# Optimization experiments

Measured on AMD Instinct MI355X. Metric: run time of the kernel, lower is better.

The kernel has to match this reference:

```python
import jax, jax.numpy as jnp
import numpy as np

B, S, DIN, D, H, DOUT, W = 4, 2048, 256, 512, 8, 128, 64
HD = D // H


def setup_inputs() -> dict:
    key = jax.random.key(0)
    ks = jax.random.split(key, 16)
    r = lambda k, shape, s=0.02: (jax.random.normal(k, shape, jnp.float32) * s)
    return dict(
        x=jax.random.normal(ks[0], (B, S, DIN), jnp.float32),
        pos=jax.random.normal(ks[1], (1, S, D), jnp.float32),  # torch.randn init
        win_w=r(ks[2], (DIN, D)), win_b=jnp.zeros((D,), jnp.float32),
        l_wqkv=r(ks[3], (3, D, D)), l_bqkv=jnp.zeros((3, D), jnp.float32),
        l_wo=r(ks[4], (D, D)), l_bo=jnp.zeros((D,), jnp.float32),
        g_wqkv=r(ks[5], (3, D, D)), g_bqkv=jnp.zeros((3, D), jnp.float32),
        g_wo=r(ks[6], (D, D)), g_bo=jnp.zeros((D,), jnp.float32),
        gate_w=r(ks[7], (2 * D, D)), gate_b=jnp.zeros((D,), jnp.float32),
        ffn_w1=r(ks[8], (D, 2 * D)), ffn_b1=jnp.zeros((2 * D,), jnp.float32),
        ffn_w2=r(ks[9], (2 * D, D)), ffn_b2=jnp.zeros((D,), jnp.float32),
        n1_g=jnp.ones((D,), jnp.float32), n1_b=jnp.zeros((D,), jnp.float32),
        n2_g=jnp.ones((D,), jnp.float32), n2_b=jnp.zeros((D,), jnp.float32),
        n3_g=jnp.ones((D,), jnp.float32), n3_b=jnp.zeros((D,), jnp.float32),
        out_w=r(ks[10], (D, DOUT)), out_b=jnp.zeros((DOUT,), jnp.float32),
    )


def _ln(x, g, b, eps=1e-5):
    m = x.mean(-1, keepdims=True)
    v = ((x - m) ** 2).mean(-1, keepdims=True)
    return (x - m) * jax.lax.rsqrt(v + eps) * g + b


def _mha(x, wqkv, bqkv, wo, bo, mask):
    b, s, d = x.shape
    q = (x @ wqkv[0] + bqkv[0]).reshape(b, s, H, HD)
    k = (x @ wqkv[1] + bqkv[1]).reshape(b, s, H, HD)
    v = (x @ wqkv[2] + bqkv[2]).reshape(b, s, H, HD)
    scores = jnp.einsum('bqhd,bkhd->bhqk', q, k) / np.sqrt(HD).astype(np.float32)
    if mask is not None:
        scores = scores + mask  # additive -inf band mask
    attn = jax.nn.softmax(scores, axis=-1)
    o = jnp.einsum('bhqk,bkhd->bqhd', attn, v).reshape(b, s, d)
    return o @ wo + bo


def reference(x, pos, win_w, win_b,
              l_wqkv, l_bqkv, l_wo, l_bo,
              g_wqkv, g_bqkv, g_wo, g_bo,
              gate_w, gate_b, ffn_w1, ffn_b1, ffn_w2, ffn_b2,
              n1_g, n1_b, n2_g, n2_b, n3_g, n3_b, out_w, out_b):
    s = x.shape[1]
    # band mask: row i allows cols [i - W//2, i + W//2] (matches create_local_mask)
    idx = jnp.arange(s)
    band = jnp.abs(idx[:, None] - idx[None, :]) <= (W // 2)
    mask = jnp.where(band, 0.0, -jnp.inf).astype(jnp.float32)

    h = x @ win_w + win_b + pos
    local_out = _mha(h, l_wqkv, l_bqkv, l_wo, l_bo, mask)
    global_out = _mha(h, g_wqkv, g_bqkv, g_wo, g_bo, None)

    combined = jnp.concatenate([local_out, global_out], axis=-1)
    gate = jnp.tanh(jax.nn.relu(combined @ gate_w + gate_b))
    fused = gate * local_out + (1.0 - gate) * global_out

    h = _ln(h + fused, n1_g, n1_b)
    ffn = jax.nn.relu(h @ ffn_w1 + ffn_b1) @ ffn_w2 + ffn_b2
    h = _ln(h + ffn, n2_g, n2_b)
    h = _ln(h, n3_g, n3_b)
    pooled = h.mean(axis=1)  # AdaptiveAvgPool1d(1) over seq
    return pooled @ out_w + out_b
```

## Files before the change

kernel.cpp:

```cpp
#include <hip/hip_runtime.h>
#include <math.h>
#include <stdint.h>

#define S_LEN 2048
#define DMODEL 512
#define NHEAD 8
#define BATCH 4
#define M_ROWS (BATCH * S_LEN)
#define UAC 4194304

typedef __attribute__((ext_vector_type(8))) short frag8;
typedef __attribute__((ext_vector_type(4))) float f32x4;

__device__ inline unsigned short f2bf(float f) {
    unsigned int u = __float_as_uint(f);
    return (unsigned short)((u + 0x7FFFu + ((u >> 16) & 1u)) >> 16);
}
__device__ inline float bf2f(unsigned short h) {
    return __uint_as_float(((unsigned int)h) << 16);
}

#if __has_builtin(__builtin_amdgcn_exp2f)
#define EXP2(x) __builtin_amdgcn_exp2f(x)
#else
#define EXP2(x) __expf(0.6931471805599453f * (x))
#endif

#if __has_builtin(__builtin_amdgcn_global_load_lds)
__device__ __forceinline__ void glds16(const void* g, void* l, int lane) {
    __builtin_amdgcn_global_load_lds(
        (__attribute__((address_space(1))) void*)(uintptr_t)g,
        (__attribute__((address_space(3))) void*)(uintptr_t)l, 16, 0, 0);
    (void)lane;
}
#else
__device__ __forceinline__ void glds16(const void* g, void* l, int lane) {
    ((uint4*)l)[lane] = ((const uint4*)g)[0];
}
#endif

struct WSeg { const float* src; unsigned short* dst; int K; int N; int start; };
struct WTab { WSeg s[12]; };

__global__ __launch_bounds__(256) void wcast_all(WTab tab)
{
    __shared__ float t[32][33];
    const int bid = blockIdx.x;
    int si = 0;
#pragma unroll
    for (int i = 1; i < 12; ++i) if (bid >= tab.s[i].start) si = i;
    const WSeg sg = tab.s[si];
    const int tile = bid - sg.start;
    const int nk = sg.K >> 5;
    const int k0 = (tile % nk) * 32, n0 = (tile / nk) * 32;
    {
        int kk = threadIdx.x >> 3, nq = (threadIdx.x & 7) * 4;
        float4 v = *(const float4*)&sg.src[(size_t)(k0 + kk) * sg.N + n0 + nq];
        t[kk][nq + 0] = v.x; t[kk][nq + 1] = v.y; t[kk][nq + 2] = v.z; t[kk][nq + 3] = v.w;
    }
    __syncthreads();
    {
        int n = threadIdx.x >> 3, kq = (threadIdx.x & 7) * 4;
        ushort4 o;
        o.x = f2bf(t[kq + 0][n]); o.y = f2bf(t[kq + 1][n]);
        o.z = f2bf(t[kq + 2][n]); o.w = f2bf(t[kq + 3][n]);
        *(ushort4*)&sg.dst[(size_t)(n0 + n) * sg.K + k0 + kq] = o;
    }
}

__global__ __launch_bounds__(256) void castx_kernel(
    const float* __restrict__ x, unsigned short* __restrict__ xb)
{
    const size_t i = ((size_t)blockIdx.x * 256 + threadIdx.x) * 8;
    float4 a = *(const float4*)&x[i], b = *(const float4*)&x[i + 4];
    unsigned short us[8];
    us[0] = f2bf(a.x); us[1] = f2bf(a.y); us[2] = f2bf(a.z); us[3] = f2bf(a.w);
    us[4] = f2bf(b.x); us[5] = f2bf(b.y); us[6] = f2bf(b.z); us[7] = f2bf(b.w);
    *(uint4*)&xb[i] = *(uint4*)us;
}

__global__ __launch_bounds__(256) void vtrans_kernel(
    const unsigned short* __restrict__ V, unsigned short* __restrict__ Vt)
{
    __shared__ unsigned short T[64][72];
    const int st = blockIdx.x, bh = blockIdx.y;
    const int b = bh >> 3, h = bh & 7;
    const int tid = threadIdx.x;
    {
        const int s = tid >> 2, d0 = (tid & 3) * 16;
        const unsigned short* src = V + ((size_t)(b * S_LEN + st * 64 + s) * DMODEL + h * 64 + d0);
        *(uint4*)&T[s][d0] = *(const uint4*)src;
        *(uint4*)&T[s][d0 + 8] = *(const uint4*)(src + 8);
    }
    __syncthreads();
    {
        const int d = tid >> 2, s0 = (tid & 3) * 16;
        unsigned short buf[16];
#pragma unroll
        for (int j = 0; j < 16; ++j) buf[j] = T[s0 + j][d];
        unsigned short* dst = Vt + ((size_t)(bh * 64 + d) * S_LEN + st * 64 + s0);
        *(uint4*)&dst[0] = *(const uint4*)&buf[0];
        *(uint4*)&dst[8] = *(const uint4*)&buf[8];
    }
}

template <int MODE, int BN>
__global__ __launch_bounds__(256) void gemm_mfma(
    const unsigned short* __restrict__ A, const unsigned short* __restrict__ A2,
    const unsigned short* __restrict__ Wt, const float* __restrict__ bias,
    const float* __restrict__ pos, unsigned short* __restrict__ C,
    int M, int N, int K)
{
    constexpr int UN = BN / 32;
    __shared__ unsigned short As[128 * 64];
    __shared__ unsigned short Bs[BN * 64];
    const int tid = threadIdx.x;
    const int wave = tid >> 6, lane = tid & 63;
    const int lr = lane & 15, quad = lane >> 4;
    const int bm = blockIdx.x * 128, bn = blockIdx.y * BN;
    const int rm = (wave >> 1) * 64, rn = (wave & 1) * (BN / 2);
    const int Khalf = K >> 1;
    const int KA = (MODE == 3) ? Khalf : K;

    const int lrow = lane >> 3;
    const int gch = ((lane & 7) - lrow) & 7;
    const size_t laneA = (size_t)(bm + wave * 32 + lrow) * KA + gch * 8;
    const size_t laneB = (size_t)(bn + wave * (BN / 4) + lrow) * K + gch * 8;
    unsigned short* ldsA = As + wave * 2048;
    unsigned short* ldsB = Bs + wave * (BN * 16);

    f32x4 acc[4][UN];
#pragma unroll
    for (int t = 0; t < 4; ++t)
#pragma unroll
        for (int u = 0; u < UN; ++u) acc[t][u] = (f32x4){0.f, 0.f, 0.f, 0.f};

    const int sw0 = ((quad + lr) & 7) * 8;
    const int sw1 = ((quad + lr + 4) & 7) * 8;

    for (int k0 = 0; k0 < K; k0 += 64) {
        __syncthreads();
        const unsigned short* Ab; int kadj;
        if constexpr (MODE == 3) { Ab = (k0 < Khalf) ? A : A2; kadj = k0 & (Khalf - 1); }
        else { Ab = A; kadj = k0; }
        const unsigned short* pa = Ab + laneA + kadj;
        glds16(pa,           ldsA,        lane);
        glds16(pa + 8 * KA,  ldsA + 512,  lane);
        glds16(pa + 16 * KA, ldsA + 1024, lane);
        glds16(pa + 24 * KA, ldsA + 1536, lane);
        const unsigned short* pb = Wt + laneB + k0;
#pragma unroll
        for (int i = 0; i < UN; ++i)
            glds16(pb + i * 8 * K, ldsB + i * 512, lane);
        __syncthreads();

#pragma unroll
        for (int kc = 0; kc < 2; ++kc) {
            const int sw = kc ? sw1 : sw0;
            frag8 af[4], bf[UN];
#pragma unroll
            for (int t = 0; t < 4; ++t)
                af[t] = *(const frag8*)&As[(rm + t * 16 + lr) * 64 + sw];
#pragma unroll
            for (int u = 0; u < UN; ++u)
                bf[u] = *(const frag8*)&Bs[(rn + u * 16 + lr) * 64 + sw];
#pragma unroll
            for (int t = 0; t < 4; ++t)
#pragma unroll
                for (int u = 0; u < UN; ++u)
                    acc[t][u] = __builtin_amdgcn_mfma_f32_16x16x32_bf16(
                        af[t], bf[u], acc[t][u], 0, 0, 0);
        }
    }

#pragma unroll
    for (int t = 0; t < 4; ++t) {
#pragma unroll
        for (int i = 0; i < 4; ++i) {
            const int m = bm + rm + t * 16 + quad * 4 + i;
#pragma unroll
            for (int u = 0; u < UN; ++u) {
                const int n = bn + rn + u * 16 + lr;
                float v = acc[t][u][i] + bias[n];
                if constexpr (MODE == 1) v += pos[(size_t)(m & (S_LEN - 1)) * N + n];
                if constexpr (MODE == 2) v = fmaxf(v, 0.0f);
                if constexpr (MODE == 3) {
                    float g = tanhf(fmaxf(v, 0.0f));
                    float lo = bf2f(A[(size_t)m * Khalf + n]);
                    float go = bf2f(A2[(size_t)m * Khalf + n]);
                    v = g * lo + (1.0f - g) * go;
                }
                if constexpr (MODE == 5) {
                    const int mat = n >> 9;
                    if (mat == 0) v *= 0.18033688011112042f;
                    C[(size_t)mat * UAC + (size_t)m * DMODEL + (n & 511)] = f2bf(v);
                } else {
                    C[(size_t)m * N + n] = f2bf(v);
                }
            }
        }
    }
}

__global__ __launch_bounds__(256) void attn_mfma(
    const unsigned short* __restrict__ Q, const unsigned short* __restrict__ Kv,
    const unsigned short* __restrict__ Vt, unsigned short* __restrict__ O, int masked)
{
    __shared__ unsigned short Ks[64 * 64];
    __shared__ unsigned short Vts[64 * 64];
    __shared__ unsigned short Ps[64][72];
    const int qt = blockIdx.x, h = blockIdx.y, b = blockIdx.z;
    const int tid = threadIdx.x;
    const int wave = tid >> 6, lane = tid & 63;
    const int lr = lane & 15, quad = lane >> 4, q8 = quad * 8;

    {
        const int q = tid >> 2, d0 = (tid & 3) * 16;
        const unsigned short* src = Q + ((size_t)(b * S_LEN + qt * 64 + q) * DMODEL + h * 64 + d0);
        *(uint4*)&Ps[q][d0] = *(const uint4*)src;
        *(uint4*)&Ps[q][d0 + 8] = *(const uint4*)(src + 8);
    }
    frag8 qf[2];
    qf[0] = *(const frag8*)&Ps[wave * 16 + lr][q8];
    qf[1] = *(const frag8*)&Ps[wave * 16 + lr][32 + q8];

    f32x4 oacc[4];
#pragma unroll
    for (int t = 0; t < 4; ++t) oacc[t] = (f32x4){0.f, 0.f, 0.f, 0.f};
    float l_r = 0.f;

    int kt0 = 0, kt1 = S_LEN / 64 - 1;
    if (masked) { kt0 = qt > 0 ? qt - 1 : 0; kt1 = qt < 31 ? qt + 1 : 31; }

    const int lrow = lane >> 3;
    const int gch = ((lane & 7) - lrow) & 7;
    const unsigned short* kp = Kv + ((size_t)(b * S_LEN + kt0 * 64 + wave * 16 + lrow) * DMODEL + h * 64 + gch * 8);
    const unsigned short* vp = Vt + ((size_t)((b * 8 + h) * 64 + wave * 16 + lrow) * S_LEN + kt0 * 64 + gch * 8);
    unsigned short* lk = Ks + wave * 1024;
    unsigned short* lv = Vts + wave * 1024;

    const int sw0 = ((quad + lr) & 7) * 8;
    const int sw1 = ((quad + lr + 4) & 7) * 8;

    for (int kt = kt0; kt <= kt1; ++kt) {
        __syncthreads();
        glds16(kp, lk, lane);
        glds16(kp + 8 * DMODEL, lk + 512, lane);
        glds16(vp, lv, lane);
        glds16(vp + 8 * S_LEN, lv + 512, lane);
        kp += 64 * DMODEL; vp += 64;
        __syncthreads();

        f32x4 sacc[4];
#pragma unroll
        for (int t = 0; t < 4; ++t) sacc[t] = (f32x4){0.f, 0.f, 0.f, 0.f};
#pragma unroll
        for (int kc = 0; kc < 2; ++kc) {
            const int sw = kc ? sw1 : sw0;
#pragma unroll
            for (int t = 0; t < 4; ++t) {
                frag8 kf = *(const frag8*)&Ks[(t * 16 + lr) * 64 + sw];
                sacc[t] = __builtin_amdgcn_mfma_f32_16x16x32_bf16(kf, qf[kc], sacc[t], 0, 0, 0);
            }
        }

#pragma unroll
        for (int t = 0; t < 4; ++t) {
            float p0 = EXP2(sacc[t][0]);
            float p1 = EXP2(sacc[t][1]);
            float p2 = EXP2(sacc[t][2]);
            float p3 = EXP2(sacc[t][3]);
            if (masked) {
                const int qa = qt * 64 + wave * 16 + lr;
                const int ca = kt * 64 + t * 16 + quad * 4;
                int d0 = qa - ca;
                if (d0 > 32 || d0 < -32) p0 = 0.f;
                int d1 = qa - (ca + 1);
                if (d1 > 32 || d1 < -32) p1 = 0.f;
                int d2 = qa - (ca + 2);
                if (d2 > 32 || d2 < -32) p2 = 0.f;
                int d3 = qa - (ca + 3);
                if (d3 > 32 || d3 < -32) p3 = 0.f;
            }
            const unsigned u0 = __float_as_uint(p0) & 0xFFFF0000u;
            const unsigned u1 = __float_as_uint(p1) & 0xFFFF0000u;
            const unsigned u2 = __float_as_uint(p2) & 0xFFFF0000u;
            const unsigned u3 = __float_as_uint(p3) & 0xFFFF0000u;
            l_r += (__uint_as_float(u0) + __uint_as_float(u1)) +
                   (__uint_as_float(u2) + __uint_as_float(u3));
            uint2 pw;
            pw.x = __builtin_amdgcn_perm(u1, u0, 0x07060302);
            pw.y = __builtin_amdgcn_perm(u3, u2, 0x07060302);
            *(uint2*)&Ps[wave * 16 + lr][t * 16 + quad * 4] = pw;
        }

#pragma unroll
        for (int cc = 0; cc < 2; ++cc) {
            frag8 pa = *(const frag8*)&Ps[wave * 16 + lr][cc * 32 + q8];
            const int sw = cc ? sw1 : sw0;
#pragma unroll
            for (int t = 0; t < 4; ++t) {
                frag8 vf = *(const frag8*)&Vts[(t * 16 + lr) * 64 + sw];
                oacc[t] = __builtin_amdgcn_mfma_f32_16x16x32_bf16(pa, vf, oacc[t], 0, 0, 0);
            }
        }
    }

    l_r += __shfl_xor(l_r, 16);
    l_r += __shfl_xor(l_r, 32);
#pragma unroll
    for (int i = 0; i < 4; ++i) {
        const float inv = 1.0f / __shfl(l_r, quad * 4 + i);
        const int q = qt * 64 + wave * 16 + quad * 4 + i;
#pragma unroll
        for (int t = 0; t < 4; ++t)
            O[(size_t)(b * S_LEN + q) * DMODEL + h * 64 + t * 16 + lr] = f2bf(oacc[t][i] * inv);
    }
}

__device__ inline float wave_sum64(float v) {
#pragma unroll
    for (int off = 1; off < 64; off <<= 1) v += __shfl_xor(v, off);
    return v;
}

__global__ __launch_bounds__(256) void ln_res_kernel(
    const unsigned short* __restrict__ A, const unsigned short* __restrict__ Bb,
    const float* __restrict__ g, const float* __restrict__ be,
    unsigned short* __restrict__ out)
{
    const size_t row = blockIdx.x * 4 + (threadIdx.x >> 6);
    const int lane = threadIdx.x & 63;
    float x[8]; float s = 0.f;
#pragma unroll
    for (int k = 0; k < 8; ++k) {
        size_t idx = row * DMODEL + k * 64 + lane;
        x[k] = bf2f(A[idx]) + bf2f(Bb[idx]);
        s += x[k];
    }
    s = wave_sum64(s);
    float mean = s * (1.0f / DMODEL);
    float v = 0.f;
#pragma unroll
    for (int k = 0; k < 8; ++k) { float d = x[k] - mean; v += d * d; }
    v = wave_sum64(v) * (1.0f / DMODEL);
    float r = rsqrtf(v + 1e-5f);
#pragma unroll
    for (int k = 0; k < 8; ++k)
        out[row * DMODEL + k * 64 + lane] =
            f2bf((x[k] - mean) * r * g[k * 64 + lane] + be[k * 64 + lane]);
}

__global__ __launch_bounds__(256) void ln_double_kernel(
    const unsigned short* __restrict__ A, const unsigned short* __restrict__ Bb,
    const float* __restrict__ g2, const float* __restrict__ b2,
    const float* __restrict__ g3, const float* __restrict__ b3,
    unsigned short* __restrict__ out)
{
    const size_t row = blockIdx.x * 4 + (threadIdx.x >> 6);
    const int lane = threadIdx.x & 63;
    float x[8]; float s = 0.f;
#pragma unroll
    for (int k = 0; k < 8; ++k) {
        size_t idx = row * DMODEL + k * 64 + lane;
        x[k] = bf2f(A[idx]) + bf2f(Bb[idx]);
        s += x[k];
    }
    s = wave_sum64(s);
    float mean = s * (1.0f / DMODEL);
    float v = 0.f;
#pragma unroll
    for (int k = 0; k < 8; ++k) { float d = x[k] - mean; v += d * d; }
    v = wave_sum64(v) * (1.0f / DMODEL);
    float r = rsqrtf(v + 1e-5f);
    float t[8]; float s2 = 0.f;
#pragma unroll
    for (int k = 0; k < 8; ++k) {
        t[k] = (x[k] - mean) * r * g2[k * 64 + lane] + b2[k * 64 + lane];
        s2 += t[k];
    }
    s2 = wave_sum64(s2);
    float mean2 = s2 * (1.0f / DMODEL);
    float v2 = 0.f;
#pragma unroll
    for (int k = 0; k < 8; ++k) { float d = t[k] - mean2; v2 += d * d; }
    v2 = wave_sum64(v2) * (1.0f / DMODEL);
    float r2 = rsqrtf(v2 + 1e-5f);
#pragma unroll
    for (int k = 0; k < 8; ++k)
        out[row * DMODEL + k * 64 + lane] =
            f2bf((t[k] - mean2) * r2 * g3[k * 64 + lane] + b3[k * 64 + lane]);
}

__global__ __launch_bounds__(256) void pool_kernel(
    const unsigned short* __restrict__ h2, float* __restrict__ pooled)
{
    const int b = blockIdx.x >> 4;
    const int chunk = blockIdx.x & 15;
    const int tid = threadIdx.x;
    float s0 = 0.f, s1 = 0.f;
    size_t base = (size_t)(b * S_LEN + chunk * 128) * DMODEL;
    for (int r = 0; r < 128; ++r) {
        s0 += bf2f(h2[base + (size_t)r * DMODEL + tid]);
        s1 += bf2f(h2[base + (size_t)r * DMODEL + 256 + tid]);
    }
    atomicAdd(&pooled[b * DMODEL + tid], s0);
    atomicAdd(&pooled[b * DMODEL + 256 + tid], s1);
}

__global__ __launch_bounds__(128) void out_kernel(
    const float* __restrict__ pooled, const float* __restrict__ w,
    const float* __restrict__ bias, float* __restrict__ out)
{
    const int b = blockIdx.x;
    const int o = threadIdx.x;
    float acc = 0.f;
    for (int d = 0; d < DMODEL; ++d)
        acc += pooled[b * DMODEL + d] * w[d * 128 + o];
    out[b * 128 + o] = acc * (1.0f / S_LEN) + bias[o];
}

extern "C" void kernel_launch(void* const* d_in, const int* in_sizes, int n_in,
                              void* d_out, int out_size, void* d_ws, size_t ws_size,
                              hipStream_t stream)
{
    const float* x      = (const float*)d_in[0];
    const float* pos    = (const float*)d_in[1];
    const float* win_w  = (const float*)d_in[2];
    const float* win_b  = (const float*)d_in[3];
    const float* l_wqkv = (const float*)d_in[4];
    const float* l_bqkv = (const float*)d_in[5];
    const float* l_wo   = (const float*)d_in[6];
    const float* l_bo   = (const float*)d_in[7];
    const float* g_wqkv = (const float*)d_in[8];
    const float* g_bqkv = (const float*)d_in[9];
    const float* g_wo   = (const float*)d_in[10];
    const float* g_bo   = (const float*)d_in[11];
    const float* gate_w = (const float*)d_in[12];
    const float* gate_b = (const float*)d_in[13];
    const float* ffn_w1 = (const float*)d_in[14];
    const float* ffn_b1 = (const float*)d_in[15];
    const float* ffn_w2 = (const float*)d_in[16];
    const float* ffn_b2 = (const float*)d_in[17];
    const float* n1_g   = (const float*)d_in[18];
    const float* n1_b   = (const float*)d_in[19];
    const float* n2_g   = (const float*)d_in[20];
    const float* n2_b   = (const float*)d_in[21];
    const float* n3_g   = (const float*)d_in[22];
    const float* n3_b   = (const float*)d_in[23];
    const float* out_w  = (const float*)d_in[24];
    const float* out_b  = (const float*)d_in[25];
    float* out = (float*)d_out;

    unsigned short* ws16 = (unsigned short*)d_ws;
    const size_t UA = (size_t)UAC;
    unsigned short* H  = ws16 + 0 * UA;
    unsigned short* Qb = ws16 + 1 * UA;
    unsigned short* Kb = ws16 + 2 * UA;
    unsigned short* Vb = ws16 + 3 * UA;
    unsigned short* AO = ws16 + 4 * UA;
    unsigned short* LO = ws16 + 5 * UA;
    unsigned short* VT = ws16 + 6 * UA;
    unsigned short* GO     = Qb;
    unsigned short* FUSED  = Kb;
    unsigned short* H1     = Vb;
    unsigned short* FFNMID = AO;
    unsigned short* FFNOUT = Qb;
    unsigned short* H2     = Kb;
    float* POOLED = (float*)(void*)H;

    unsigned short* wt = ws16 + 7 * UA;
    unsigned short* win_t  = wt;
    unsigned short* lqkv_t = win_t  + 131072;
    unsigned short* lwo_t  = lqkv_t + 786432;
    unsigned short* gqkv_t = lwo_t  + 262144;
    unsigned short* gwo_t  = gqkv_t + 786432;
    unsigned short* gate_t = gwo_t  + 262144;
    unsigned short* ffn1_t = gate_t + 524288;
    unsigned short* ffn2_t = ffn1_t + 524288;
    unsigned short* xb     = ffn2_t + 524288;

    WTab tab;
    tab.s[0]  = {win_w,             win_t,             256,  512,    0};
    tab.s[1]  = {l_wqkv + 0*262144, lqkv_t + 0*262144, 512,  512,  128};
    tab.s[2]  = {l_wqkv + 1*262144, lqkv_t + 1*262144, 512,  512,  384};
    tab.s[3]  = {l_wqkv + 2*262144, lqkv_t + 2*262144, 512,  512,  640};
    tab.s[4]  = {l_wo,              lwo_t,             512,  512,  896};
    tab.s[5]  = {g_wqkv + 0*262144, gqkv_t + 0*262144, 512,  512, 1152};
    tab.s[6]  = {g_wqkv + 1*262144, gqkv_t + 1*262144, 512,  512, 1408};
    tab.s[7]  = {g_wqkv + 2*262144, gqkv_t + 2*262144, 512,  512, 1664};
    tab.s[8]  = {g_wo,              gwo_t,             512,  512, 1920};
    tab.s[9]  = {gate_w,            gate_t,            1024, 512, 2176};
    tab.s[10] = {ffn_w1,            ffn1_t,            512, 1024, 2688};
    tab.s[11] = {ffn_w2,            ffn2_t,            1024, 512, 3200};

    dim3 blk(256);
    wcast_all<<<dim3(3712), blk, 0, stream>>>(tab);
    castx_kernel<<<dim3(1024), blk, 0, stream>>>(x, xb);

    dim3 gD(M_ROWS / 128, 512 / 64);
    dim3 gQ(M_ROWS / 128, 1536 / 128);
    dim3 gF(M_ROWS / 128, 1024 / 128);
    dim3 gA(S_LEN / 64, NHEAD, BATCH);
    dim3 gV(S_LEN / 64, BATCH * NHEAD);

    gemm_mfma<1, 64><<<gD, blk, 0, stream>>>(xb, nullptr, win_t, win_b, pos, H, M_ROWS, 512, 256);

    gemm_mfma<5, 128><<<gQ, blk, 0, stream>>>(H, nullptr, lqkv_t, l_bqkv, nullptr, Qb, M_ROWS, 1536, 512);
    vtrans_kernel<<<gV, blk, 0, stream>>>(Vb, VT);
    attn_mfma<<<gA, blk, 0, stream>>>(Qb, Kb, VT, AO, 1);
    gemm_mfma<0, 64><<<gD, blk, 0, stream>>>(AO, nullptr, lwo_t, l_bo, nullptr, LO, M_ROWS, 512, 512);

    gemm_mfma<5, 128><<<gQ, blk, 0, stream>>>(H, nullptr, gqkv_t, g_bqkv, nullptr, Qb, M_ROWS, 1536, 512);
    vtrans_kernel<<<gV, blk, 0, stream>>>(Vb, VT);
    attn_mfma<<<gA, blk, 0, stream>>>(Qb, Kb, VT, AO, 0);
    gemm_mfma<0, 64><<<gD, blk, 0, stream>>>(AO, nullptr, gwo_t, g_bo, nullptr, GO, M_ROWS, 512, 512);

    gemm_mfma<3, 64><<<gD, blk, 0, stream>>>(LO, GO, gate_t, gate_b, nullptr, FUSED, M_ROWS, 512, 1024);

    ln_res_kernel<<<M_ROWS / 4, blk, 0, stream>>>(H, FUSED, n1_g, n1_b, H1);

    gemm_mfma<2, 128><<<gF, blk, 0, stream>>>(H1, nullptr, ffn1_t, ffn_b1, nullptr, FFNMID, M_ROWS, 1024, 512);
    gemm_mfma<0, 64><<<gD, blk, 0, stream>>>(FFNMID, nullptr, ffn2_t, ffn_b2, nullptr, FFNOUT, M_ROWS, 512, 1024);

    ln_double_kernel<<<M_ROWS / 4, blk, 0, stream>>>(H1, FFNOUT, n2_g, n2_b, n3_g, n3_b, H2);

    hipMemsetAsync(POOLED, 0, BATCH * DMODEL * sizeof(float), stream);
    pool_kernel<<<dim3(BATCH * 16), blk, 0, stream>>>(H2, POOLED);
    out_kernel<<<dim3(BATCH), dim3(128), 0, stream>>>(POOLED, out_w, out_b, out);
}
```

Baseline: 373.8 us.

## Batch local/global QKV and out-proj GEMMs; double-buffer attention K/V loads

Merges the local and global QKV projections into one wide GEMM (N=3072) and the two output projections into a single launch using blockIdx.z to choose the operand set. Attention now double-buffers the K/V tiles in LDS, prefetching the next tile while computing the current one, and uses a swizzled unpadded P/Q buffer. The goal is fewer launches, larger grids, and hiding global-load latency in attention. The cost is more LDS per attention block (lower occupancy) and an extra workspace buffer.

```diff
diff --git a/kernel.cpp b/kernel.cpp
--- a/kernel.cpp
+++ b/kernel.cpp
@@ -108,7 +108,8 @@
 __global__ __launch_bounds__(256) void gemm_mfma(
     const unsigned short* __restrict__ A, const unsigned short* __restrict__ A2,
     const unsigned short* __restrict__ Wt, const float* __restrict__ bias,
-    const float* __restrict__ pos, unsigned short* __restrict__ C,
+    const float* __restrict__ bias2, const float* __restrict__ pos,
+    unsigned short* __restrict__ C, unsigned short* __restrict__ C2,
     int M, int N, int K)
 {
     constexpr int UN = BN / 32;
@@ -122,6 +123,14 @@
     const int Khalf = K >> 1;
     const int KA = (MODE == 3) ? Khalf : K;
 
+    const unsigned short* SA = A;
+    const unsigned short* SW = Wt;
+    const float* SBIAS = bias;
+    unsigned short* SC = C;
+    if constexpr (MODE == 6) {
+        if (blockIdx.z) { SA = A2; SW = Wt + 512 * 512; SBIAS = bias2; SC = C2; }
+    }
+
     const int lrow = lane >> 3;
     const int gch = ((lane & 7) - lrow) & 7;
     const size_t laneA = (size_t)(bm + wave * 32 + lrow) * KA + gch * 8;
@@ -142,13 +151,13 @@
         __syncthreads();
         const unsigned short* Ab; int kadj;
         if constexpr (MODE == 3) { Ab = (k0 < Khalf) ? A : A2; kadj = k0 & (Khalf - 1); }
-        else { Ab = A; kadj = k0; }
+        else { Ab = SA; kadj = k0; }
         const unsigned short* pa = Ab + laneA + kadj;
         glds16(pa,           ldsA,        lane);
         glds16(pa + 8 * KA,  ldsA + 512,  lane);
         glds16(pa + 16 * KA, ldsA + 1024, lane);
         glds16(pa + 24 * KA, ldsA + 1536, lane);
-        const unsigned short* pb = Wt + laneB + k0;
+        const unsigned short* pb = SW + laneB + k0;
 #pragma unroll
         for (int i = 0; i < UN; ++i)
             glds16(pb + i * 8 * K, ldsB + i * 512, lane);
@@ -181,48 +190,64 @@
 #pragma unroll
             for (int u = 0; u < UN; ++u) {
                 const int n = bn + rn + u * 16 + lr;
-                float v = acc[t][u][i] + bias[n];
-                if constexpr (MODE == 1) v += pos[(size_t)(m & (S_LEN - 1)) * N + n];
-                if constexpr (MODE == 2) v = fmaxf(v, 0.0f);
-                if constexpr (MODE == 3) {
-                    float g = tanhf(fmaxf(v, 0.0f));
-                    float lo = bf2f(A[(size_t)m * Khalf + n]);
-                    float go = bf2f(A2[(size_t)m * Khalf + n]);
-                    v = g * lo + (1.0f - g) * go;
-                }
                 if constexpr (MODE == 5) {
                     const int mat = n >> 9;
-                    if (mat == 0) v *= 0.18033688011112042f;
-                    C[(size_t)mat * UAC + (size_t)m * DMODEL + (n & 511)] = f2bf(v);
+                    const int nn = n & 511;
+                    const float* bp = (mat < 3) ? (bias + (mat << 9))
+                                                : (bias2 + ((mat - 3) << 9));
+                    float v = acc[t][u][i] + bp[nn];
+                    if (mat == 0 || mat == 3) v *= 0.18033688011112042f;
+                    C[(size_t)mat * UAC + (size_t)m * DMODEL + nn] = f2bf(v);
                 } else {
-                    C[(size_t)m * N + n] = f2bf(v);
+                    float v = acc[t][u][i] + SBIAS[n];
+                    if constexpr (MODE == 1) v += pos[(size_t)(m & (S_LEN - 1)) * N + n];
+                    if constexpr (MODE == 2) v = fmaxf(v, 0.0f);
+                    if constexpr (MODE == 3) {
+                        float g = tanhf(fmaxf(v, 0.0f));
+                        float lo = bf2f(A[(size_t)m * Khalf + n]);
+                        float go = bf2f(A2[(size_t)m * Khalf + n]);
+                        v = g * lo + (1.0f - g) * go;
+                    }
+                    SC[(size_t)m * N + n] = f2bf(v);
                 }
             }
         }
     }
 }
 
+#define ISSUE_KV(KT, BUF) do {                                                  \
+    const unsigned short* _kp = kbase + (size_t)(KT) * (64 * DMODEL);           \
+    const unsigned short* _vp = vbase + (size_t)(KT) * 64;                      \
+    unsigned short* _lk = Ks + (BUF) * 4096 + wave * 1024;                      \
+    unsigned short* _lv = Vts + (BUF) * 4096 + wave * 1024;                     \
+    glds16(_kp, _lk, lane); glds16(_kp + 8 * DMODEL, _lk + 512, lane);          \
+    glds16(_vp, _lv, lane); glds16(_vp + 8 * S_LEN, _lv + 512, lane);           \
+} while (0)
+
 __global__ __launch_bounds__(256) void attn_mfma(
     const unsigned short* __restrict__ Q, const unsigned short* __restrict__ Kv,
     const unsigned short* __restrict__ Vt, unsigned short* __restrict__ O, int masked)
 {
-    __shared__ unsigned short Ks[64 * 64];
-    __shared__ unsigned short Vts[64 * 64];
-    __shared__ unsigned short Ps[64][72];
+    __shared__ unsigned short Ks[2 * 64 * 64];
+    __shared__ unsigned short Vts[2 * 64 * 64];
+    __shared__ unsigned short Ps[64 * 64];
     const int qt = blockIdx.x, h = blockIdx.y, b = blockIdx.z;
     const int tid = threadIdx.x;
     const int wave = tid >> 6, lane = tid & 63;
-    const int lr = lane & 15, quad = lane >> 4, q8 = quad * 8;
+    const int lr = lane & 15, quad = lane >> 4;
 
     {
-        const int q = tid >> 2, d0 = (tid & 3) * 16;
-        const unsigned short* src = Q + ((size_t)(b * S_LEN + qt * 64 + q) * DMODEL + h * 64 + d0);
-        *(uint4*)&Ps[q][d0] = *(const uint4*)src;
-        *(uint4*)&Ps[q][d0 + 8] = *(const uint4*)(src + 8);
-    }
+        const int q = tid >> 2, c8 = (tid & 3) * 2;
+        const unsigned short* src = Q + ((size_t)(b * S_LEN + qt * 64 + q) * DMODEL + h * 64 + c8 * 8);
+        *(uint4*)&Ps[q * 64 + (((c8 + q) & 7) * 8)] = *(const uint4*)src;
+        *(uint4*)&Ps[q * 64 + (((c8 + 1 + q) & 7) * 8)] = *(const uint4*)(src + 8);
+    }
+    const int sw0 = ((quad + lr) & 7) * 8;
+    const int sw1 = ((quad + lr + 4) & 7) * 8;
+    const int prow = (wave * 16 + lr) * 64;
     frag8 qf[2];
-    qf[0] = *(const frag8*)&Ps[wave * 16 + lr][q8];
-    qf[1] = *(const frag8*)&Ps[wave * 16 + lr][32 + q8];
+    qf[0] = *(const frag8*)&Ps[prow + sw0];
+    qf[1] = *(const frag8*)&Ps[prow + sw1];
 
     f32x4 oacc[4];
 #pragma unroll
@@ -231,25 +256,22 @@
 
     int kt0 = 0, kt1 = S_LEN / 64 - 1;
     if (masked) { kt0 = qt > 0 ? qt - 1 : 0; kt1 = qt < 31 ? qt + 1 : 31; }
+    const int nt = kt1 - kt0 + 1;
 
     const int lrow = lane >> 3;
     const int gch = ((lane & 7) - lrow) & 7;
-    const unsigned short* kp = Kv + ((size_t)(b * S_LEN + kt0 * 64 + wave * 16 + lrow) * DMODEL + h * 64 + gch * 8);
-    const unsigned short* vp = Vt + ((size_t)((b * 8 + h) * 64 + wave * 16 + lrow) * S_LEN + kt0 * 64 + gch * 8);
-    unsigned short* lk = Ks + wave * 1024;
-    unsigned short* lv = Vts + wave * 1024;
-
-    const int sw0 = ((quad + lr) & 7) * 8;
-    const int sw1 = ((quad + lr + 4) & 7) * 8;
-
-    for (int kt = kt0; kt <= kt1; ++kt) {
+    const unsigned short* kbase = Kv + ((size_t)(b * S_LEN + kt0 * 64 + wave * 16 + lrow) * DMODEL + h * 64 + gch * 8);
+    const unsigned short* vbase = Vt + ((size_t)((b * 8 + h) * 64 + wave * 16 + lrow) * S_LEN + kt0 * 64 + gch * 8);
+
+    ISSUE_KV(0, 0);
+
+    for (int it = 0; it < nt; ++it) {
+        const int buf = it & 1;
         __syncthreads();
-        glds16(kp, lk, lane);
-        glds16(kp + 8 * DMODEL, lk + 512, lane);
-        glds16(vp, lv, lane);
-        glds16(vp + 8 * S_LEN, lv + 512, lane);
-        kp += 64 * DMODEL; vp += 64;
-        __syncthreads();
+        if (it + 1 < nt) ISSUE_KV(it + 1, buf ^ 1);
+
+        const unsigned short* kb = Ks + buf * 4096;
+        const unsigned short* vb = Vts + buf * 4096;
 
         f32x4 sacc[4];
 #pragma unroll
@@ -259,11 +281,12 @@
             const int sw = kc ? sw1 : sw0;
 #pragma unroll
             for (int t = 0; t < 4; ++t) {
-                frag8 kf = *(const frag8*)&Ks[(t * 16 + lr) * 64 + sw];
+                frag8 kf = *(const frag8*)&kb[(t * 16 + lr) * 64 + sw];
                 sacc[t] = __builtin_amdgcn_mfma_f32_16x16x32_bf16(kf, qf[kc], sacc[t], 0, 0, 0);
             }
         }
 
+        const int kt = kt0 + it;
 #pragma unroll
         for (int t = 0; t < 4; ++t) {
             float p0 = EXP2(sacc[t][0]);
@@ -291,16 +314,17 @@
             uint2 pw;
             pw.x = __builtin_amdgcn_perm(u1, u0, 0x07060302);
             pw.y = __builtin_amdgcn_perm(u3, u2, 0x07060302);
-            *(uint2*)&Ps[wave * 16 + lr][t * 16 + quad * 4] = pw;
+            const int slot = ((2 * t + (quad >> 1) + lr) & 7) * 8 + (quad & 1) * 4;
+            *(uint2*)&Ps[prow + slot] = pw;
         }
 
 #pragma unroll
         for (int cc = 0; cc < 2; ++cc) {
-            frag8 pa = *(const frag8*)&Ps[wave * 16 + lr][cc * 32 + q8];
             const int sw = cc ? sw1 : sw0;
+            frag8 pa = *(const frag8*)&Ps[prow + sw];
 #pragma unroll
             for (int t = 0; t < 4; ++t) {
-                frag8 vf = *(const frag8*)&Vts[(t * 16 + lr) * 64 + sw];
+                frag8 vf = *(const frag8*)&vb[(t * 16 + lr) * 64 + sw];
                 oacc[t] = __builtin_amdgcn_mfma_f32_16x16x32_bf16(pa, vf, oacc[t], 0, 0, 0);
             }
         }
@@ -454,27 +478,32 @@
 
     unsigned short* ws16 = (unsigned short*)d_ws;
     const size_t UA = (size_t)UAC;
-    unsigned short* H  = ws16 + 0 * UA;
-    unsigned short* Qb = ws16 + 1 * UA;
-    unsigned short* Kb = ws16 + 2 * UA;
-    unsigned short* Vb = ws16 + 3 * UA;
-    unsigned short* AO = ws16 + 4 * UA;
-    unsigned short* LO = ws16 + 5 * UA;
-    unsigned short* VT = ws16 + 6 * UA;
-    unsigned short* GO     = Qb;
-    unsigned short* FUSED  = Kb;
-    unsigned short* H1     = Vb;
-    unsigned short* FFNMID = AO;
-    unsigned short* FFNOUT = Qb;
-    unsigned short* H2     = Kb;
+    unsigned short* H    = ws16 + 0 * UA;
+    unsigned short* QKV  = ws16 + 1 * UA;
+    unsigned short* Ql   = ws16 + 1 * UA;
+    unsigned short* Kl   = ws16 + 2 * UA;
+    unsigned short* Vl   = ws16 + 3 * UA;
+    unsigned short* Qg   = ws16 + 4 * UA;
+    unsigned short* Kg   = ws16 + 5 * UA;
+    unsigned short* Vg   = ws16 + 6 * UA;
+    unsigned short* VT   = ws16 + 7 * UA;
+    unsigned short* AOl    = Vl;
+    unsigned short* AOg    = Ql;
+    unsigned short* LO     = Kl;
+    unsigned short* GO     = Qg;
+    unsigned short* FUSED  = Kg;
+    unsigned short* H1     = Vg;
+    unsigned short* FFNMID = Vl;
+    unsigned short* FFNOUT = Ql;
+    unsigned short* H2     = Kl;
     float* POOLED = (float*)(void*)H;
 
-    unsigned short* wt = ws16 + 7 * UA;
+    unsigned short* wt = ws16 + 8 * UA;
     unsigned short* win_t  = wt;
     unsigned short* lqkv_t = win_t  + 131072;
-    unsigned short* lwo_t  = lqkv_t + 786432;
-    unsigned short* gqkv_t = lwo_t  + 262144;
-    unsigned short* gwo_t  = gqkv_t + 786432;
+    unsigned short* gqkv_t = lqkv_t + 786432;
+    unsigned short* lwo_t  = gqkv_t + 786432;
+    unsigned short* gwo_t  = lwo_t  + 262144;
     unsigned short* gate_t = gwo_t  + 262144;
     unsigned short* ffn1_t = gate_t + 524288;
     unsigned short* ffn2_t = ffn1_t + 524288;
@@ -485,10 +514,10 @@
     tab.s[1]  = {l_wqkv + 0*262144, lqkv_t + 0*262144, 512,  512,  128};
     tab.s[2]  = {l_wqkv + 1*262144, lqkv_t + 1*262144, 512,  512,  384};
     tab.s[3]  = {l_wqkv + 2*262144, lqkv_t + 2*262144, 512,  512,  640};
-    tab.s[4]  = {l_wo,              lwo_t,             512,  512,  896};
-    tab.s[5]  = {g_wqkv + 0*262144, gqkv_t + 0*262144, 512,  512, 1152};
-    tab.s[6]  = {g_wqkv + 1*262144, gqkv_t + 1*262144, 512,  512, 1408};
-    tab.s[7]  = {g_wqkv + 2*262144, gqkv_t + 2*262144, 512,  512, 1664};
+    tab.s[4]  = {g_wqkv + 0*262144, gqkv_t + 0*262144, 512,  512,  896};
+    tab.s[5]  = {g_wqkv + 1*262144, gqkv_t + 1*262144, 512,  512, 1152};
+    tab.s[6]  = {g_wqkv + 2*262144, gqkv_t + 2*262144, 512,  512, 1408};
+    tab.s[7]  = {l_wo,              lwo_t,             512,  512, 1664};
     tab.s[8]  = {g_wo,              gwo_t,             512,  512, 1920};
     tab.s[9]  = {gate_w,            gate_t,            1024, 512, 2176};
     tab.s[10] = {ffn_w1,            ffn1_t,            512, 1024, 2688};
@@ -499,29 +528,29 @@
     castx_kernel<<<dim3(1024), blk, 0, stream>>>(x, xb);
 
     dim3 gD(M_ROWS / 128, 512 / 64);
-    dim3 gQ(M_ROWS / 128, 1536 / 128);
+    dim3 gW(M_ROWS / 128, 512 / 64, 2);
+    dim3 gQ(M_ROWS / 128, 3072 / 128);
     dim3 gF(M_ROWS / 128, 1024 / 128);
     dim3 gA(S_LEN / 64, NHEAD, BATCH);
     dim3 gV(S_LEN / 64, BATCH * NHEAD);
 
-    gemm_mfma<1, 64><<<gD, blk, 0, stream>>>(xb, nullptr, win_t, win_b, pos, H, M_ROWS, 512, 256);
-
-    gemm_mfma<5, 128><<<gQ, blk, 0, stream>>>(H, nullptr, lqkv_t, l_bqkv, nullptr, Qb, M_ROWS, 1536, 512);
-    vtrans_kernel<<<gV, blk, 0, stream>>>(Vb, VT);
-    attn_mfma<<<gA, blk, 0, stream>>>(Qb, Kb, VT, AO, 1);
-    gemm_mfma<0, 64><<<gD, blk, 0, stream>>>(AO, nullptr, lwo_t, l_bo, nullptr, LO, M_ROWS, 512, 512);
-
-    gemm_mfma<5, 128><<<gQ, blk, 0, stream>>>(H, nullptr, gqkv_t, g_bqkv, nullptr, Qb, M_ROWS, 1536, 512);
-    vtrans_kernel<<<gV, blk, 0, stream>>>(Vb, VT);
-    attn_mfma<<<gA, blk, 0, stream>>>(Qb, Kb, VT, AO, 0);
-    gemm_mfma<0, 64><<<gD, blk, 0, stream>>>(AO, nullptr, gwo_t, g_bo, nullptr, GO, M_ROWS, 512, 512);
-
-    gemm_mfma<3, 64><<<gD, blk, 0, stream>>>(LO, GO, gate_t, gate_b, nullptr, FUSED, M_ROWS, 512, 1024);
+    gemm_mfma<1, 64><<<gD, blk, 0, stream>>>(xb, nullptr, win_t, win_b, nullptr, pos, H, nullptr, M_ROWS, 512, 256);
+
+    gemm_mfma<5, 128><<<gQ, blk, 0, stream>>>(H, nullptr, lqkv_t, l_bqkv, g_bqkv, nullptr, QKV, nullptr, M_ROWS, 3072, 512);
+
+    vtrans_kernel<<<gV, blk, 0, stream>>>(Vl, VT);
+    attn_mfma<<<gA, blk, 0, stream>>>(Ql, Kl, VT, AOl, 1);
+    vtrans_kernel<<<gV, blk, 0, stream>>>(Vg, VT);
+    attn_mfma<<<gA, blk, 0, stream>>>(Qg, Kg, VT, AOg, 0);
+
+    gemm_mfma<6, 64><<<gW, blk, 0, stream>>>(AOl, AOg, lwo_t, l_bo, g_bo, nullptr, LO, GO, M_ROWS, 512, 512);
+
+    gemm_mfma<3, 64><<<gD, blk, 0, stream>>>(LO, GO, gate_t, gate_b, nullptr, nullptr, FUSED, nullptr, M_ROWS, 512, 1024);
 
     ln_res_kernel<<<M_ROWS / 4, blk, 0, stream>>>(H, FUSED, n1_g, n1_b, H1);
 
-    gemm_mfma<2, 128><<<gF, blk, 0, stream>>>(H1, nullptr, ffn1_t, ffn_b1, nullptr, FFNMID, M_ROWS, 1024, 512);
-    gemm_mfma<0, 64><<<gD, blk, 0, stream>>>(FFNMID, nullptr, ffn2_t, ffn_b2, nullptr, FFNOUT, M_ROWS, 512, 1024);
+    gemm_mfma<2, 128><<<gF, blk, 0, stream>>>(H1, nullptr, ffn1_t, ffn_b1, nullptr, nullptr, FFNMID, nullptr, M_ROWS, 1024, 512);
+    gemm_mfma<0, 64><<<gD, blk, 0, stream>>>(FFNMID, nullptr, ffn2_t, ffn_b2, nullptr, nullptr, FFNOUT, nullptr, M_ROWS, 512, 1024);
 
     ln_double_kernel<<<M_ROWS / 4, blk, 0, stream>>>(H1, FFNOUT, n2_g, n2_b, n3_g, n3_b, H2);
 
```

Result: faster. 358.6 us (-4.1%).
